# Performance work log

Measured on AMD Instinct MI355X. Metric: run time of the kernel, lower is better.

The kernel has to match this reference:

```python
import jax, jax.numpy as jnp
import numpy as np

N_NODES = 50000
N_EDGES = 800000
IN_CH = 128
HID = 64
OUT_CH = 2
N_GRAPHS = 512


def gcn_conv(x, edge_index, W, b, num_nodes):
    # PyG GCNConv: h = x @ W, add self-loops, sym-normalize, scatter-add, add bias
    loop = jnp.arange(num_nodes, dtype=edge_index.dtype)
    src = jnp.concatenate([edge_index[0], loop])
    dst = jnp.concatenate([edge_index[1], loop])
    deg = jax.ops.segment_sum(jnp.ones_like(dst, dtype=x.dtype), dst, num_segments=num_nodes)
    dinv = jnp.where(deg > 0, jax.lax.rsqrt(deg), 0.0)
    norm = dinv[src] * dinv[dst]                      # [E+N]
    h = x @ W                                         # [N, HID]
    msg = h[src] * norm[:, None]                      # gather + scale
    out = jax.ops.segment_sum(msg, dst, num_segments=num_nodes)  # scatter-add
    return out + b


def global_mean_pool(x, batch, num_graphs):
    s = jax.ops.segment_sum(x, batch, num_segments=num_graphs)
    cnt = jax.ops.segment_sum(jnp.ones((x.shape[0],), x.dtype), batch, num_segments=num_graphs)
    return s / jnp.maximum(cnt, 1.0)[:, None]


def setup_inputs() -> dict:
    key = jax.random.key(0)
    ks = jax.random.split(key, 9)
    x = jax.random.normal(ks[0], (N_NODES, IN_CH), dtype=jnp.float32)
    edge_index = jax.random.randint(ks[1], (2, N_EDGES), 0, N_NODES, dtype=jnp.int64)
    batch = jnp.sort(jax.random.randint(ks[2], (N_NODES,), 0, N_GRAPHS, dtype=jnp.int64))
    W1 = jax.random.normal(ks[3], (IN_CH, HID), dtype=jnp.float32) * (1.0 / np.sqrt(IN_CH))
    b1 = jnp.zeros((HID,), dtype=jnp.float32)
    W2 = jax.random.normal(ks[4], (HID, HID), dtype=jnp.float32) * (1.0 / np.sqrt(HID))
    b2 = jnp.zeros((HID,), dtype=jnp.float32)
    Wl = jax.random.normal(ks[5], (HID, OUT_CH), dtype=jnp.float32) * (1.0 / np.sqrt(HID))
    bl = jnp.zeros((OUT_CH,), dtype=jnp.float32)
    return {"x": x, "edge_index": edge_index, "batch": batch,
            "W1": W1, "b1": b1, "W2": W2, "b2": b2, "Wl": Wl, "bl": bl}


def reference(x, edge_index, batch, W1, b1, W2, b2, Wl, bl):
    h = jax.nn.relu(gcn_conv(x, edge_index, W1, b1, N_NODES))
    h = jax.nn.relu(gcn_conv(h, edge_index, W2, b2, N_NODES))
    g = global_mean_pool(h, batch, N_GRAPHS)          # [N_GRAPHS, HID]
    return g @ Wl + bl                                # [N_GRAPHS, OUT_CH]
```

## Files before the change

### kernel.cpp

```cpp
#include <hip/hip_runtime.h>

constexpr int HID = 64;
constexpr int RB = 128;
constexpr int KC = 32;
constexpr int NPB = 128;
constexpr int MAXBUCK = 512;
constexpr int CAP = 2560;
constexpr int CHUNK = 2048;

__global__ __launch_bounds__(256) void k_bucket(const int* __restrict__ src,
                                                const int* __restrict__ dst, int nE,
                                                int* __restrict__ bcursor,
                                                int2* __restrict__ pairs, int nBuck) {
  __shared__ int hist[MAXBUCK];
  __shared__ int base[MAXBUCK];
  const int t = threadIdx.x;
  const int e0 = blockIdx.x * CHUNK;
  const int eEnd = min(e0 + CHUNK, nE);
  for (int i = t; i < nBuck; i += 256) hist[i] = 0;
  __syncthreads();
  for (int e = e0 + t; e < eEnd; e += 256)
    atomicAdd(&hist[dst[e] >> 7], 1);
  __syncthreads();
  for (int i = t; i < nBuck; i += 256) {
    int c = hist[i];
    int r = (c > 0) ? atomicAdd(&bcursor[i], c) : 0;
    base[i] = i * CAP + r;
    hist[i] = 0;
  }
  __syncthreads();
  for (int e = e0 + t; e < eEnd; e += 256) {
    int d = dst[e];
    int b = d >> 7;
    int idx = atomicAdd(&hist[b], 1);
    pairs[base[b] + idx] = make_int2(src[e], d);
  }
}

__global__ __launch_bounds__(256) void k_place(const int2* __restrict__ pairs,
                                               const int* __restrict__ bcursor,
                                               int* __restrict__ csr,
                                               int* __restrict__ row_lo,
                                               int* __restrict__ row_hi,
                                               float* __restrict__ dinv, int nN) {
  __shared__ int cnt[NPB], sc[NPB], cur[NPB];
  const int t = threadIdx.x;
  const int b = blockIdx.x;
  const int vbase = b * NPB;
  const int lo = b * CAP;
  const int npairs = bcursor[b];
  if (t < NPB) cnt[t] = 0;
  __syncthreads();
  for (int p = t; p < npairs; p += 256)
    atomicAdd(&cnt[pairs[lo + p].y - vbase], 1);
  __syncthreads();
  if (t < NPB) sc[t] = cnt[t];
  __syncthreads();
  for (int d = 1; d < NPB; d <<= 1) {
    int x = 0;
    if (t < NPB) { x = sc[t]; if (t >= d) x += sc[t - d]; }
    __syncthreads();
    if (t < NPB) sc[t] = x;
    __syncthreads();
  }
  if (t < NPB && vbase + t < nN) {
    int ex = sc[t] - cnt[t];
    row_lo[vbase + t] = lo + ex;
    row_hi[vbase + t] = lo + sc[t];
    dinv[vbase + t] = rsqrtf((float)cnt[t] + 1.0f);
    cur[t] = lo + ex;
  }
  __syncthreads();
  for (int p = t; p < npairs; p += 256) {
    int2 e = pairs[lo + p];
    int pos = atomicAdd(&cur[e.y - vbase], 1);
    csr[pos] = e.x;
  }
}

template <int K>
__global__ __launch_bounds__(256) void k_mm_tile(const float* __restrict__ X,
                                                 const float* __restrict__ W,
                                                 const float* __restrict__ dinv,
                                                 float* __restrict__ out, int nRows) {
  __shared__ float Xs[RB][KC + 1];
  __shared__ float Ws[KC][HID];

  const int t    = threadIdx.x;
  const int lane = t & 63;
  const int wid  = t >> 6;
  const int rg   = lane >> 3;
  const int cg   = lane & 7;
  const int rb   = blockIdx.x * RB;
  const int rloc = wid * 32 + rg * 4;

  float acc[4][8];
#pragma unroll
  for (int i = 0; i < 4; ++i)
#pragma unroll
    for (int j = 0; j < 8; ++j) acc[i][j] = 0.f;

  for (int c = 0; c < K / KC; ++c) {
    const int k0 = c * KC;
    {
      const int r  = t >> 1;
      const int kh = (t & 1) * 16;
      const int grow = rb + r;
      if (grow < nRows) {
        const float* p = X + (size_t)grow * K + k0 + kh;
#pragma unroll
        for (int q = 0; q < 4; ++q) {
          const float4 v = *(const float4*)(p + q * 4);
          float* d = &Xs[r][kh + q * 4];
          d[0] = v.x; d[1] = v.y; d[2] = v.z; d[3] = v.w;
        }
      }
    }
    {
      const float* p = W + (size_t)(k0 + (t >> 3)) * HID + (t & 7) * 8;
      const float4 v0 = *(const float4*)p;
      const float4 v1 = *(const float4*)(p + 4);
      float* d = &Ws[t >> 3][(t & 7) * 8];
      ((float4*)d)[0] = v0;
      ((float4*)d)[1] = v1;
    }
    __syncthreads();

#pragma unroll
    for (int k = 0; k < KC; ++k) {
      const float4 w0 = *(const float4*)&Ws[k][cg * 8];
      const float4 w1 = *(const float4*)&Ws[k][cg * 8 + 4];
      float xv[4];
#pragma unroll
      for (int i = 0; i < 4; ++i) xv[i] = Xs[rloc + i][k];
#pragma unroll
      for (int i = 0; i < 4; ++i) {
        acc[i][0] = fmaf(xv[i], w0.x, acc[i][0]);
        acc[i][1] = fmaf(xv[i], w0.y, acc[i][1]);
        acc[i][2] = fmaf(xv[i], w0.z, acc[i][2]);
        acc[i][3] = fmaf(xv[i], w0.w, acc[i][3]);
        acc[i][4] = fmaf(xv[i], w1.x, acc[i][4]);
        acc[i][5] = fmaf(xv[i], w1.y, acc[i][5]);
        acc[i][6] = fmaf(xv[i], w1.z, acc[i][6]);
        acc[i][7] = fmaf(xv[i], w1.w, acc[i][7]);
      }
    }
    __syncthreads();
  }

#pragma unroll
  for (int i = 0; i < 4; ++i) {
    const int row = rb + rloc + i;
    if (row < nRows) {
      const float s = dinv[row];
      float4 o0, o1;
      o0.x = acc[i][0] * s; o0.y = acc[i][1] * s; o0.z = acc[i][2] * s; o0.w = acc[i][3] * s;
      o1.x = acc[i][4] * s; o1.y = acc[i][5] * s; o1.z = acc[i][6] * s; o1.w = acc[i][7] * s;
      float* p = out + (size_t)row * HID + cg * 8;
      ((float4*)p)[0] = o0;
      ((float4*)p)[1] = o1;
    }
  }
}

__global__ __launch_bounds__(256) void k_gather_mm(const int* __restrict__ csr,
                                                   const int* __restrict__ row_lo,
                                                   const int* __restrict__ row_hi,
                                                   const float4* __restrict__ H4,
                                                   const float* __restrict__ dinv,
                                                   const float* __restrict__ b,
                                                   const float* __restrict__ W2,
                                                   float4* __restrict__ out4, int nN) {
  __shared__ float W2s[HID][HID];
  __shared__ float z1s[16][68];

  const int t = threadIdx.x;
  for (int i = t; i < HID * HID / 4; i += 256)
    ((float4*)W2s)[i] = ((const float4*)W2)[i];
  __syncthreads();

  const int wid = t >> 6;
  const int lane = t & 63;
  const int ng = lane >> 4;
  const int cq = lane & 15;
  const int nl = wid * 4 + ng;
  const int v = blockIdx.x * 16 + nl;
  const int vv = min(v, nN - 1);
  const int lo = row_lo[vv];
  const int cnt = row_hi[vv] - lo;

  double acc[4][4];
#pragma unroll
  for (int c = 0; c < 4; ++c)
#pragma unroll
    for (int q = 0; q < 4; ++q) acc[c][q] = 0.0;
  {
    const float4 sv = H4[(size_t)vv * 16 + cq];
    acc[0][0] = (double)sv.x; acc[0][1] = (double)sv.y;
    acc[0][2] = (double)sv.z; acc[0][3] = (double)sv.w;
  }

  for (int base = 0; base < cnt; base += 16) {
    int idxv = (base + cq < cnt) ? csr[lo + base + cq] : 0;
#pragma unroll
    for (int j = 0; j < 16; ++j) {
      int s = __shfl(idxv, (ng << 4) + j, 64);
      if (base + j < cnt) {
        const float4 h = H4[(size_t)s * 16 + cq];
        acc[j & 3][0] += (double)h.x;
        acc[j & 3][1] += (double)h.y;
        acc[j & 3][2] += (double)h.z;
        acc[j & 3][3] += (double)h.w;
      }
    }
  }

  {
    const float dv = dinv[vv];
    const float4 bb = ((const float4*)b)[cq];
    float4 z;
    z.x = fmaxf(fmaf(dv, (float)((acc[0][0] + acc[1][0]) + (acc[2][0] + acc[3][0])), bb.x), 0.f);
    z.y = fmaxf(fmaf(dv, (float)((acc[0][1] + acc[1][1]) + (acc[2][1] + acc[3][1])), bb.y), 0.f);
    z.z = fmaxf(fmaf(dv, (float)((acc[0][2] + acc[1][2]) + (acc[2][2] + acc[3][2])), bb.z), 0.f);
    z.w = fmaxf(fmaf(dv, (float)((acc[0][3] + acc[1][3]) + (acc[2][3] + acc[3][3])), bb.w), 0.f);
    float* zp = &z1s[nl][cq * 4];
    zp[0] = z.x; zp[1] = z.y; zp[2] = z.z; zp[3] = z.w;
  }

  float h0 = 0.f, h1 = 0.f, h2 = 0.f, h3 = 0.f;
#pragma unroll 8
  for (int k = 0; k < HID; ++k) {
    const float zk = z1s[nl][k];
    const float4 w = *(const float4*)&W2s[k][cq * 4];
    h0 = fmaf(zk, w.x, h0);
    h1 = fmaf(zk, w.y, h1);
    h2 = fmaf(zk, w.z, h2);
    h3 = fmaf(zk, w.w, h3);
  }

  if (v < nN) {
    const float dv = dinv[v];
    float4 o;
    o.x = h0 * dv; o.y = h1 * dv; o.z = h2 * dv; o.w = h3 * dv;
    out4[(size_t)v * 16 + cq] = o;
  }
}

__global__ __launch_bounds__(256) void k_gather4(const int* __restrict__ csr,
                                                 const int* __restrict__ row_lo,
                                                 const int* __restrict__ row_hi,
                                                 const float4* __restrict__ H4,
                                                 const float* __restrict__ dinv,
                                                 const float* __restrict__ b,
                                                 float4* __restrict__ out4, int nN) {
  const int t = threadIdx.x;
  const int wid = t >> 6;
  const int lane = t & 63;
  const int ng = lane >> 4;
  const int cq = lane & 15;
  const int v = blockIdx.x * 16 + wid * 4 + ng;
  const int vv = min(v, nN - 1);
  const int lo = row_lo[vv];
  const int cnt = row_hi[vv] - lo;

  double acc[4][4];
#pragma unroll
  for (int c = 0; c < 4; ++c)
#pragma unroll
    for (int q = 0; q < 4; ++q) acc[c][q] = 0.0;
  {
    const float4 sv = H4[(size_t)vv * 16 + cq];
    acc[0][0] = (double)sv.x; acc[0][1] = (double)sv.y;
    acc[0][2] = (double)sv.z; acc[0][3] = (double)sv.w;
  }

  for (int base = 0; base < cnt; base += 16) {
    int idxv = (base + cq < cnt) ? csr[lo + base + cq] : 0;
#pragma unroll
    for (int j = 0; j < 16; ++j) {
      int s = __shfl(idxv, (ng << 4) + j, 64);
      if (base + j < cnt) {
        const float4 h = H4[(size_t)s * 16 + cq];
        acc[j & 3][0] += (double)h.x;
        acc[j & 3][1] += (double)h.y;
        acc[j & 3][2] += (double)h.z;
        acc[j & 3][3] += (double)h.w;
      }
    }
  }

  if (v < nN) {
    const float dv = dinv[v];
    const float4 bb = ((const float4*)b)[cq];
    float4 o;
    o.x = fmaxf(fmaf(dv, (float)((acc[0][0] + acc[1][0]) + (acc[2][0] + acc[3][0])), bb.x), 0.f);
    o.y = fmaxf(fmaf(dv, (float)((acc[0][1] + acc[1][1]) + (acc[2][1] + acc[3][1])), bb.y), 0.f);
    o.z = fmaxf(fmaf(dv, (float)((acc[0][2] + acc[1][2]) + (acc[2][2] + acc[3][2])), bb.z), 0.f);
    o.w = fmaxf(fmaf(dv, (float)((acc[0][3] + acc[1][3]) + (acc[2][3] + acc[3][3])), bb.w), 0.f);
    out4[(size_t)v * 16 + cq] = o;
  }
}

__device__ inline int lowerb(const int* __restrict__ a, int n, int key) {
  int lo = 0, hi = n;
  while (lo < hi) {
    int mid = (lo + hi) >> 1;
    if (a[mid] < key) lo = mid + 1; else hi = mid;
  }
  return lo;
}

__global__ __launch_bounds__(256) void k_pool_head(const float* __restrict__ Z,
                                                   const int* __restrict__ batch, int nN,
                                                   const float* __restrict__ Wl,
                                                   const float* __restrict__ bl,
                                                   float* __restrict__ out) {
  int g = blockIdx.x;
  int lane = threadIdx.x & 63;
  int wid = threadIdx.x >> 6;
  int lo = lowerb(batch, nN, g);
  int hi = lowerb(batch, nN, g + 1);
  double acc = 0.0;
  for (int r = lo + wid; r < hi; r += 4) acc += (double)Z[(size_t)r * HID + lane];
  __shared__ double s[4][HID];
  s[wid][lane] = acc;
  __syncthreads();
  if (wid == 0) {
    double tot = (s[0][lane] + s[1][lane]) + (s[2][lane] + s[3][lane]);
    double mean = tot / (double)max(hi - lo, 1);
    double p0 = mean * (double)Wl[lane * 2 + 0];
    double p1 = mean * (double)Wl[lane * 2 + 1];
#pragma unroll
    for (int off = 32; off; off >>= 1) {
      p0 += __shfl_xor(p0, off, 64);
      p1 += __shfl_xor(p1, off, 64);
    }
    if (lane == 0) {
      out[g * 2 + 0] = (float)(p0 + (double)bl[0]);
      out[g * 2 + 1] = (float)(p1 + (double)bl[1]);
    }
  }
}

extern "C" void kernel_launch(void* const* d_in, const int* in_sizes, int n_in,
                              void* d_out, int out_size, void* d_ws, size_t ws_size,
                              hipStream_t stream) {
  const float* x     = (const float*)d_in[0];
  const int*   ei    = (const int*)d_in[1];
  const int*   batch = (const int*)d_in[2];
  const float* W1    = (const float*)d_in[3];
  const float* b1    = (const float*)d_in[4];
  const float* W2    = (const float*)d_in[5];
  const float* b2    = (const float*)d_in[6];
  const float* Wl    = (const float*)d_in[7];
  const float* bl    = (const float*)d_in[8];
  float* out = (float*)d_out;

  const int nN = in_sizes[2];
  const int nE = in_sizes[1] / 2;
  const int nG = out_size / 2;
  const int* src = ei;
  const int* dst = ei + nE;

  char* ws = (char*)d_ws;
  size_t off = 0;
  auto alloc = [&](size_t bytes) {
    char* p = ws + off;
    off += (bytes + 255) & ~(size_t)255;
    return p;
  };
  int*   bcursor = (int*)alloc(MAXBUCK * 4);
  int*   row_lo  = (int*)alloc((size_t)nN * 4);
  int*   row_hi  = (int*)alloc((size_t)nN * 4);
  int*   csr     = (int*)alloc((size_t)MAXBUCK * CAP * 4);
  float* dinv    = (float*)alloc((size_t)nN * 4);
  float* A       = (float*)alloc((size_t)nN * HID * 4);
  float* B       = (float*)alloc((size_t)nN * HID * 4);
  int2*  pairs   = (int2*)A;

  const int nBuck = (nN + NPB - 1) / NPB;

  hipMemsetAsync(bcursor, 0, MAXBUCK * 4, stream);
  k_bucket<<<(nE + CHUNK - 1) / CHUNK, 256, 0, stream>>>(src, dst, nE, bcursor, pairs, nBuck);
  k_place<<<nBuck, 256, 0, stream>>>(pairs, bcursor, csr, row_lo, row_hi, dinv, nN);

  k_mm_tile<128><<<(nN + RB - 1) / RB, 256, 0, stream>>>(x, W1, dinv, A, nN);

  k_gather_mm<<<(nN + 15) / 16, 256, 0, stream>>>(csr, row_lo, row_hi, (const float4*)A,
                                                  dinv, b1, W2, (float4*)B, nN);

  k_gather4<<<(nN + 15) / 16, 256, 0, stream>>>(csr, row_lo, row_hi, (const float4*)B,
                                                dinv, b2, (float4*)A, nN);

  k_pool_head<<<nG, 256, 0, stream>>>(A, batch, nN, Wl, bl, out);
}
```

Baseline: 140.1 us.

## Fuse mean-pool into second gather via double atomics and prefetch CSR indices

```diff
diff --git a/kernel.cpp b/kernel.cpp
--- a/kernel.cpp
+++ b/kernel.cpp
@@ -11,7 +11,11 @@
 __global__ __launch_bounds__(256) void k_bucket(const int* __restrict__ src,
                                                 const int* __restrict__ dst, int nE,
                                                 int* __restrict__ bcursor,
-                                                int2* __restrict__ pairs, int nBuck) {
+                                                int2* __restrict__ pairs, int nBuck,
+                                                double* __restrict__ gsumd, int gsumN) {
+  for (int i = blockIdx.x * 256 + threadIdx.x; i < gsumN; i += gridDim.x * 256)
+    gsumd[i] = 0.0;
+
   __shared__ int hist[MAXBUCK];
   __shared__ int base[MAXBUCK];
   const int t = threadIdx.x;
@@ -200,8 +204,10 @@
     acc[0][2] = (double)sv.z; acc[0][3] = (double)sv.w;
   }
 
+  int idxv = (cq < cnt) ? csr[lo + cq] : 0;
   for (int base = 0; base < cnt; base += 16) {
-    int idxv = (base + cq < cnt) ? csr[lo + base + cq] : 0;
+    const int nb = base + 16;
+    int nidx = (nb + cq < cnt) ? csr[lo + nb + cq] : 0;
 #pragma unroll
     for (int j = 0; j < 16; ++j) {
       int s = __shfl(idxv, (ng << 4) + j, 64);
@@ -213,6 +219,7 @@
         acc[j & 3][3] += (double)h.w;
       }
     }
+    idxv = nidx;
   }
 
   {
@@ -246,13 +253,14 @@
   }
 }
 
-__global__ __launch_bounds__(256) void k_gather4(const int* __restrict__ csr,
-                                                 const int* __restrict__ row_lo,
-                                                 const int* __restrict__ row_hi,
-                                                 const float4* __restrict__ H4,
-                                                 const float* __restrict__ dinv,
-                                                 const float* __restrict__ b,
-                                                 float4* __restrict__ out4, int nN) {
+__global__ __launch_bounds__(256) void k_gather_pool(const int* __restrict__ csr,
+                                                     const int* __restrict__ row_lo,
+                                                     const int* __restrict__ row_hi,
+                                                     const float4* __restrict__ H4,
+                                                     const float* __restrict__ dinv,
+                                                     const float* __restrict__ b,
+                                                     const int* __restrict__ batch,
+                                                     double* __restrict__ gsumd, int nN) {
   const int t = threadIdx.x;
   const int wid = t >> 6;
   const int lane = t & 63;
@@ -274,8 +282,10 @@
     acc[0][2] = (double)sv.z; acc[0][3] = (double)sv.w;
   }
 
+  int idxv = (cq < cnt) ? csr[lo + cq] : 0;
   for (int base = 0; base < cnt; base += 16) {
-    int idxv = (base + cq < cnt) ? csr[lo + base + cq] : 0;
+    const int nb = base + 16;
+    int nidx = (nb + cq < cnt) ? csr[lo + nb + cq] : 0;
 #pragma unroll
     for (int j = 0; j < 16; ++j) {
       int s = __shfl(idxv, (ng << 4) + j, 64);
@@ -287,17 +297,22 @@
         acc[j & 3][3] += (double)h.w;
       }
     }
+    idxv = nidx;
   }
 
   if (v < nN) {
     const float dv = dinv[v];
     const float4 bb = ((const float4*)b)[cq];
-    float4 o;
-    o.x = fmaxf(fmaf(dv, (float)((acc[0][0] + acc[1][0]) + (acc[2][0] + acc[3][0])), bb.x), 0.f);
-    o.y = fmaxf(fmaf(dv, (float)((acc[0][1] + acc[1][1]) + (acc[2][1] + acc[3][1])), bb.y), 0.f);
-    o.z = fmaxf(fmaf(dv, (float)((acc[0][2] + acc[1][2]) + (acc[2][2] + acc[3][2])), bb.z), 0.f);
-    o.w = fmaxf(fmaf(dv, (float)((acc[0][3] + acc[1][3]) + (acc[2][3] + acc[3][3])), bb.w), 0.f);
-    out4[(size_t)v * 16 + cq] = o;
+    float4 z;
+    z.x = fmaxf(fmaf(dv, (float)((acc[0][0] + acc[1][0]) + (acc[2][0] + acc[3][0])), bb.x), 0.f);
+    z.y = fmaxf(fmaf(dv, (float)((acc[0][1] + acc[1][1]) + (acc[2][1] + acc[3][1])), bb.y), 0.f);
+    z.z = fmaxf(fmaf(dv, (float)((acc[0][2] + acc[1][2]) + (acc[2][2] + acc[3][2])), bb.z), 0.f);
+    z.w = fmaxf(fmaf(dv, (float)((acc[0][3] + acc[1][3]) + (acc[2][3] + acc[3][3])), bb.w), 0.f);
+    double* gp = gsumd + (size_t)batch[v] * HID + cq * 4;
+    atomicAdd(gp + 0, (double)z.x);
+    atomicAdd(gp + 1, (double)z.y);
+    atomicAdd(gp + 2, (double)z.z);
+    atomicAdd(gp + 3, (double)z.w);
   }
 }
 
@@ -310,35 +325,28 @@
   return lo;
 }
 
-__global__ __launch_bounds__(256) void k_pool_head(const float* __restrict__ Z,
-                                                   const int* __restrict__ batch, int nN,
-                                                   const float* __restrict__ Wl,
-                                                   const float* __restrict__ bl,
-                                                   float* __restrict__ out) {
-  int g = blockIdx.x;
-  int lane = threadIdx.x & 63;
-  int wid = threadIdx.x >> 6;
-  int lo = lowerb(batch, nN, g);
-  int hi = lowerb(batch, nN, g + 1);
-  double acc = 0.0;
-  for (int r = lo + wid; r < hi; r += 4) acc += (double)Z[(size_t)r * HID + lane];
-  __shared__ double s[4][HID];
-  s[wid][lane] = acc;
-  __syncthreads();
-  if (wid == 0) {
-    double tot = (s[0][lane] + s[1][lane]) + (s[2][lane] + s[3][lane]);
-    double mean = tot / (double)max(hi - lo, 1);
-    double p0 = mean * (double)Wl[lane * 2 + 0];
-    double p1 = mean * (double)Wl[lane * 2 + 1];
-#pragma unroll
-    for (int off = 32; off; off >>= 1) {
-      p0 += __shfl_xor(p0, off, 64);
-      p1 += __shfl_xor(p1, off, 64);
-    }
-    if (lane == 0) {
-      out[g * 2 + 0] = (float)(p0 + (double)bl[0]);
-      out[g * 2 + 1] = (float)(p1 + (double)bl[1]);
-    }
+__global__ __launch_bounds__(256) void k_head(const double* __restrict__ gsumd,
+                                              const int* __restrict__ batch, int nN,
+                                              const float* __restrict__ Wl,
+                                              const float* __restrict__ bl,
+                                              float* __restrict__ out, int nG) {
+  const int wid = threadIdx.x >> 6;
+  const int lane = threadIdx.x & 63;
+  const int g = blockIdx.x * 4 + wid;
+  if (g >= nG) return;
+  const int lo = lowerb(batch, nN, g);
+  const int hi = lowerb(batch, nN, g + 1);
+  const double mean = gsumd[(size_t)g * HID + lane] / (double)max(hi - lo, 1);
+  double p0 = mean * (double)Wl[lane * 2 + 0];
+  double p1 = mean * (double)Wl[lane * 2 + 1];
+#pragma unroll
+  for (int off = 32; off; off >>= 1) {
+    p0 += __shfl_xor(p0, off, 64);
+    p1 += __shfl_xor(p1, off, 64);
+  }
+  if (lane == 0) {
+    out[g * 2 + 0] = (float)(p0 + (double)bl[0]);
+    out[g * 2 + 1] = (float)(p1 + (double)bl[1]);
   }
 }
 
@@ -369,19 +377,21 @@
     off += (bytes + 255) & ~(size_t)255;
     return p;
   };
-  int*   bcursor = (int*)alloc(MAXBUCK * 4);
-  int*   row_lo  = (int*)alloc((size_t)nN * 4);
-  int*   row_hi  = (int*)alloc((size_t)nN * 4);
-  int*   csr     = (int*)alloc((size_t)MAXBUCK * CAP * 4);
-  float* dinv    = (float*)alloc((size_t)nN * 4);
-  float* A       = (float*)alloc((size_t)nN * HID * 4);
-  float* B       = (float*)alloc((size_t)nN * HID * 4);
-  int2*  pairs   = (int2*)A;
+  int*    bcursor = (int*)alloc(MAXBUCK * 4);
+  int*    row_lo  = (int*)alloc((size_t)nN * 4);
+  int*    row_hi  = (int*)alloc((size_t)nN * 4);
+  int*    csr     = (int*)alloc((size_t)MAXBUCK * CAP * 4);
+  float*  dinv    = (float*)alloc((size_t)nN * 4);
+  double* gsumd   = (double*)alloc((size_t)nG * HID * 8);
+  float*  A       = (float*)alloc((size_t)nN * HID * 4);
+  float*  B       = (float*)alloc((size_t)nN * HID * 4);
+  int2*   pairs   = (int2*)A;
 
   const int nBuck = (nN + NPB - 1) / NPB;
 
   hipMemsetAsync(bcursor, 0, MAXBUCK * 4, stream);
-  k_bucket<<<(nE + CHUNK - 1) / CHUNK, 256, 0, stream>>>(src, dst, nE, bcursor, pairs, nBuck);
+  k_bucket<<<(nE + CHUNK - 1) / CHUNK, 256, 0, stream>>>(src, dst, nE, bcursor, pairs,
+                                                         nBuck, gsumd, nG * HID);
   k_place<<<nBuck, 256, 0, stream>>>(pairs, bcursor, csr, row_lo, row_hi, dinv, nN);
 
   k_mm_tile<128><<<(nN + RB - 1) / RB, 256, 0, stream>>>(x, W1, dinv, A, nN);
@@ -389,8 +399,8 @@
   k_gather_mm<<<(nN + 15) / 16, 256, 0, stream>>>(csr, row_lo, row_hi, (const float4*)A,
                                                   dinv, b1, W2, (float4*)B, nN);
 
-  k_gather4<<<(nN + 15) / 16, 256, 0, stream>>>(csr, row_lo, row_hi, (const float4*)B,
-                                                dinv, b2, (float4*)A, nN);
-
-  k_pool_head<<<nG, 256, 0, stream>>>(A, batch, nN, Wl, bl, out);
-}
+  k_gather_pool<<<(nN + 15) / 16, 256, 0, stream>>>(csr, row_lo, row_hi, (const float4*)B,
+                                                    dinv, b2, batch, gsumd, nN);
+
+  k_head<<<(nG + 3) / 4, 256, 0, stream>>>(gsumd, batch, nN, Wl, bl, out, nG);
+}
```

After: 211.9 us. 51.2% more time.
